# Kernel optimization log

Measured on AMD Instinct MI355X. Metric: run time of the kernel, lower is better.

## Reference

```python
import jax, jax.numpy as jnp
import numpy as np

C = 256  # hidden_channels
N = 262144  # number of nodes


def setup_inputs() -> dict:
    key = jax.random.key(0)
    ks = jax.random.split(key, 6)
    s = 1.0 / np.sqrt(C)
    return {
        "x": jax.random.normal(ks[0], (N, C), dtype=jnp.float32),
        "Wq": jax.random.uniform(ks[1], (C, C), jnp.float32, -s, s),
        "Wk": jax.random.uniform(ks[2], (C, C), jnp.float32, -s, s),
        "Wv": jax.random.uniform(ks[3], (C, C), jnp.float32, -s, s),
        "Wo": jax.random.uniform(ks[4], (C, C), jnp.float32, -s, s),
        "bo": jax.random.uniform(ks[5], (C,), jnp.float32, -s, s),
    }


def reference(x, Wq, Wk, Wv, Wo, bo):
    # torch nn.Linear: y = x @ W.T
    q = jax.nn.elu(x @ Wq.T) + 1.0          # [N, C], strictly positive feature map
    k = jax.nn.elu(x @ Wk.T) + 1.0          # [N, C]
    v = x @ Wv.T                             # [N, C]
    kv = k.T @ v                             # [C, C] aggregate
    z = 1.0 / jnp.maximum(q @ k.sum(axis=0), 1e-6)  # [N] normalizer
    h = (q @ kv) * z[:, None]                # [N, C]
    # dropout p=0.0 (and eval mode) -> identity
    return h @ Wo.T + bo
```

## Files before the change

### kernel.cpp

```cpp
#include <hip/hip_runtime.h>
#include <cstdint>


typedef __attribute__((ext_vector_type(8))) short short8;
typedef __attribute__((ext_vector_type(4))) float f32x4;
typedef unsigned short u16;
typedef unsigned int u32;

#define MFMA16(a, b, c) __builtin_amdgcn_mfma_f32_16x16x32_bf16(a, b, c, 0, 0, 0)

__device__ __forceinline__ u32 bf16_1(float f) {
  u32 u = __float_as_uint(f);
  return (u + 0x7FFFu + ((u >> 16) & 1u)) >> 16;
}
__device__ __forceinline__ u32 bf16pk(float lo, float hi) {
  return bf16_1(lo) | (bf16_1(hi) << 16);
}

__global__ void prep_kernel(const float* __restrict__ Wq, const float* __restrict__ Wk,
                            const float* __restrict__ Wv, u16* __restrict__ WqF,
                            u16* __restrict__ WkF, u16* __restrict__ WvF,
                            float* __restrict__ kvp, float* __restrict__ ksum, int P) {
  int id = blockIdx.x * 256 + threadIdx.x;
  if (id < 256) ksum[id] = 0.f;
  for (int t = id; t < 3 * 65536; t += 65536) {
    int mat = t >> 16;
    int e = t & 65535;
    int c = e >> 8, d = e & 255;
    const float* src = (mat == 0) ? Wq : (mat == 1) ? Wk : Wv;
    u16* dst = (mat == 0) ? WqF : (mat == 1) ? WkF : WvF;
    int idx = (((c >> 5) * 8 + (d >> 5)) * 2 + ((c >> 4) & 1)) * 512 +
              ((d >> 3) & 3) * 128 + (c & 15) * 8 + (d & 7);
    dst[idx] = (u16)bf16_1(src[e]);
  }
  if (P < 256) {
    float4 z4 = {0.f, 0.f, 0.f, 0.f};
    float4* kz = (float4*)kvp;
    int total = P * 16384;
    for (int t = id; t < total; t += 65536) kz[t] = z4;
  }
}

__global__ __launch_bounds__(512, 2) void phase1_kernel(
    const float* __restrict__ x, const u16* __restrict__ WkF,
    const u16* __restrict__ WvF, float* __restrict__ kvp, float* __restrict__ ksum,
    int P) {
  __shared__ __align__(16) u16 xv_l[16384];
  __shared__ __align__(16) u16 kT_l[16384];
  const int tid = threadIdx.x;
  const int lane = tid & 63;
  const int w = tid >> 6;
  const int m = lane & 15;
  const int q = lane >> 4;
  const int wg = blockIdx.x;

  const f32x4 fz = {0.f, 0.f, 0.f, 0.f};
  f32x4 kvacc[16][2];
#pragma unroll
  for (int tr = 0; tr < 16; ++tr) {
    kvacc[tr][0] = fz;
    kvacc[tr][1] = fz;
  }
  float ksl0 = 0.f, ksl1 = 0.f;

  for (int it = 0; it < 16; ++it) {
    const int row0 = wg * 1024 + it * 64;
    __syncthreads();
    {
      const int r = tid >> 3, a = tid & 7;
      const float4* xp = (const float4*)(x + (size_t)(row0 + r) * 256 + a * 32);
#pragma unroll
      for (int i = 0; i < 8; ++i) {
        float4 f = xp[i];
        int db = 4 * a + (i >> 1);
        int pos = db * 512 + ((r ^ (db & 7)) << 3) + 4 * (i & 1);
        uint2 v;
        v.x = bf16pk(f.x, f.y);
        v.y = bf16pk(f.z, f.w);
        *(uint2*)&xv_l[pos] = v;
      }
    }
    __syncthreads();
    f32x4 kacc[4][2], vacc[4][2];
#pragma unroll
    for (int rt = 0; rt < 4; ++rt) {
      kacc[rt][0] = fz; kacc[rt][1] = fz;
      vacc[rt][0] = fz; vacc[rt][1] = fz;
    }
#pragma unroll
    for (int ks = 0; ks < 8; ++ks) {
      const int fb = ((w * 8 + ks) * 2) * 512 + lane * 8;
      short8 wk0 = *(const short8*)(WkF + fb);
      short8 wk1 = *(const short8*)(WkF + fb + 512);
      short8 wv0 = *(const short8*)(WvF + fb);
      short8 wv1 = *(const short8*)(WvF + fb + 512);
      const int db = 4 * ks + q;
      const int sw = db & 7;
#pragma unroll
      for (int rt = 0; rt < 4; ++rt) {
        int r = 16 * rt + m;
        short8 af = *(const short8*)&xv_l[db * 512 + ((r ^ sw) << 3)];
        kacc[rt][0] = MFMA16(af, wk0, kacc[rt][0]);
        kacc[rt][1] = MFMA16(af, wk1, kacc[rt][1]);
        vacc[rt][0] = MFMA16(af, wv0, vacc[rt][0]);
        vacc[rt][1] = MFMA16(af, wv1, vacc[rt][1]);
      }
    }
    __syncthreads();
#pragma unroll
    for (int rt = 0; rt < 4; ++rt) {
#pragma unroll
      for (int ct = 0; ct < 2; ++ct) {
        f32x4 kk = kacc[rt][ct];
        float e0 = kk[0] > 0.f ? kk[0] + 1.f : __expf(kk[0]);
        float e1 = kk[1] > 0.f ? kk[1] + 1.f : __expf(kk[1]);
        float e2 = kk[2] > 0.f ? kk[2] + 1.f : __expf(kk[2]);
        float e3 = kk[3] > 0.f ? kk[3] + 1.f : __expf(kk[3]);
        if (ct == 0) ksl0 += (e0 + e1) + (e2 + e3);
        else         ksl1 += (e0 + e1) + (e2 + e3);
        int col = 32 * w + 16 * ct + m;
        int pos = (2 * rt + (q >> 1)) * 2048 + col * 8 + 4 * (q & 1);
        uint2 kp;
        kp.x = bf16pk(e0, e1);
        kp.y = bf16pk(e2, e3);
        *(uint2*)&kT_l[pos] = kp;
        f32x4 vv = vacc[rt][ct];
        uint2 vp;
        vp.x = bf16pk(vv[0], vv[1]);
        vp.y = bf16pk(vv[2], vv[3]);
        *(uint2*)&xv_l[pos] = vp;
      }
    }
    __syncthreads();
#pragma unroll
    for (int kc = 0; kc < 2; ++kc) {
      const int rbb = (4 * kc + q) * 2048;
      short8 bf0 = *(const short8*)&xv_l[rbb + (32 * w + m) * 8];
      short8 bf1 = *(const short8*)&xv_l[rbb + (32 * w + 16 + m) * 8];
#pragma unroll
      for (int tr = 0; tr < 16; ++tr) {
        short8 af = *(const short8*)&kT_l[rbb + (16 * tr + m) * 8];
        kvacc[tr][0] = MFMA16(af, bf0, kvacc[tr][0]);
        kvacc[tr][1] = MFMA16(af, bf1, kvacc[tr][1]);
      }
    }
  }
  float s0 = ksl0, s1 = ksl1;
  s0 += __shfl_xor(s0, 16); s0 += __shfl_xor(s0, 32);
  s1 += __shfl_xor(s1, 16); s1 += __shfl_xor(s1, 32);
  if (q == 0) {
    atomicAdd(&ksum[32 * w + m], s0);
    atomicAdd(&ksum[32 * w + 16 + m], s1);
  }
  float* dst = kvp + (size_t)((P == 256) ? wg : (wg & (P - 1))) * 65536;
  if (P == 256) {
#pragma unroll
    for (int tr = 0; tr < 16; ++tr)
#pragma unroll
      for (int ct = 0; ct < 2; ++ct)
#pragma unroll
        for (int e = 0; e < 4; ++e) {
          int i = 16 * tr + 4 * q + e;
          int j = 32 * w + 16 * ct + m;
          dst[i * 256 + j] = kvacc[tr][ct][e];
        }
  } else {
#pragma unroll
    for (int tr = 0; tr < 16; ++tr)
#pragma unroll
      for (int ct = 0; ct < 2; ++ct)
#pragma unroll
        for (int e = 0; e < 4; ++e) {
          int i = 16 * tr + 4 * q + e;
          int j = 32 * w + 16 * ct + m;
          atomicAdd(&dst[i * 256 + j], kvacc[tr][ct][e]);
        }
  }
}

__global__ void mid1_kernel(const float* __restrict__ kvp, float* __restrict__ kv_red,
                            int P) {
  int id = blockIdx.x * 512 + threadIdx.x;
  float s = 0.f;
  for (int p = 0; p < P; ++p) s += kvp[(size_t)p * 65536 + id];
  kv_red[id] = s;
}

__global__ void mid2_kernel(const float* __restrict__ kv_red,
                            const float* __restrict__ Wo, u16* __restrict__ MF) {
  __shared__ float kr[256];
  const int i = blockIdx.x;
  const int j = threadIdx.x;
  kr[j] = kv_red[i * 256 + j];
  __syncthreads();
  float acc = 0.f;
  const float* wo = Wo + (size_t)j * 256;
#pragma unroll 8
  for (int c = 0; c < 256; ++c) acc += kr[c] * wo[c];
  MF[(((j >> 5) * 8 + (i >> 5)) * 2 + ((j >> 4) & 1)) * 512 + ((i >> 3) & 3) * 128 +
     (j & 15) * 8 + (i & 7)] = (u16)bf16_1(acc);
}

__global__ __launch_bounds__(512, 2) void phase2_kernel(
    const float* __restrict__ x, const u16* __restrict__ WqF,
    const u16* __restrict__ MF, const float* __restrict__ ksum,
    const float* __restrict__ bo, float* __restrict__ out) {
  __shared__ __align__(16) u16 xq_l[16384];
  __shared__ float s_l[64];
  const int tid = threadIdx.x;
  const int lane = tid & 63;
  const int w = tid >> 6;
  const int m = lane & 15;
  const int q = lane >> 4;
  const int wg = blockIdx.x;
  const f32x4 fz = {0.f, 0.f, 0.f, 0.f};

  short8 mf[8][2];
#pragma unroll
  for (int ks = 0; ks < 8; ++ks) {
    mf[ks][0] = *(const short8*)(MF + ((w * 8 + ks) * 2) * 512 + lane * 8);
    mf[ks][1] = *(const short8*)(MF + ((w * 8 + ks) * 2 + 1) * 512 + lane * 8);
  }
  const float ks0 = ksum[32 * w + m];
  const float ks1 = ksum[32 * w + 16 + m];
  const float b0 = bo[32 * w + m];
  const float b1 = bo[32 * w + 16 + m];

  for (int it = 0; it < 16; ++it) {
    const int row0 = wg * 1024 + it * 64;
    __syncthreads();
    {
      const int r = tid >> 3, a = tid & 7;
      const float4* xp = (const float4*)(x + (size_t)(row0 + r) * 256 + a * 32);
#pragma unroll
      for (int i = 0; i < 8; ++i) {
        float4 f = xp[i];
        int db = 4 * a + (i >> 1);
        int pos = db * 512 + ((r ^ (db & 7)) << 3) + 4 * (i & 1);
        uint2 v;
        v.x = bf16pk(f.x, f.y);
        v.y = bf16pk(f.z, f.w);
        *(uint2*)&xq_l[pos] = v;
      }
      if (tid < 64) s_l[tid] = 0.f;
    }
    __syncthreads();
    f32x4 qacc[4][2];
#pragma unroll
    for (int rt = 0; rt < 4; ++rt) { qacc[rt][0] = fz; qacc[rt][1] = fz; }
#pragma unroll
    for (int ks = 0; ks < 8; ++ks) {
      const int fb = ((w * 8 + ks) * 2) * 512 + lane * 8;
      short8 wq0 = *(const short8*)(WqF + fb);
      short8 wq1 = *(const short8*)(WqF + fb + 512);
      const int db = 4 * ks + q;
      const int sw = db & 7;
#pragma unroll
      for (int rt = 0; rt < 4; ++rt) {
        int r = 16 * rt + m;
        short8 af = *(const short8*)&xq_l[db * 512 + ((r ^ sw) << 3)];
        qacc[rt][0] = MFMA16(af, wq0, qacc[rt][0]);
        qacc[rt][1] = MFMA16(af, wq1, qacc[rt][1]);
      }
    }
#pragma unroll
    for (int rt = 0; rt < 4; ++rt) {
#pragma unroll
      for (int ct = 0; ct < 2; ++ct) {
        f32x4 a = qacc[rt][ct];
        a[0] = a[0] > 0.f ? a[0] + 1.f : __expf(a[0]);
        a[1] = a[1] > 0.f ? a[1] + 1.f : __expf(a[1]);
        a[2] = a[2] > 0.f ? a[2] + 1.f : __expf(a[2]);
        a[3] = a[3] > 0.f ? a[3] + 1.f : __expf(a[3]);
        qacc[rt][ct] = a;
      }
#pragma unroll
      for (int e = 0; e < 4; ++e) {
        float val = qacc[rt][0][e] * ks0 + qacc[rt][1][e] * ks1;
        val += __shfl_xor(val, 1);
        val += __shfl_xor(val, 2);
        val += __shfl_xor(val, 4);
        val += __shfl_xor(val, 8);
        if (m == 0) atomicAdd(&s_l[16 * rt + 4 * q + e], val);
      }
    }
    __syncthreads();
#pragma unroll
    for (int rt = 0; rt < 4; ++rt)
#pragma unroll
      for (int ct = 0; ct < 2; ++ct) {
        int c = 32 * w + 16 * ct + m;
        int db = c >> 3;
        int sw = db & 7;
        int cw = c & 7;
#pragma unroll
        for (int e = 0; e < 4; ++e) {
          int r = 16 * rt + 4 * q + e;
          xq_l[db * 512 + ((r ^ sw) << 3) + cw] = (u16)bf16_1(qacc[rt][ct][e]);
        }
      }
    __syncthreads();
    f32x4 tacc[4][2];
#pragma unroll
    for (int rt = 0; rt < 4; ++rt) { tacc[rt][0] = fz; tacc[rt][1] = fz; }
#pragma unroll
    for (int ks = 0; ks < 8; ++ks) {
      const int db = 4 * ks + q;
      const int sw = db & 7;
#pragma unroll
      for (int rt = 0; rt < 4; ++rt) {
        int r = 16 * rt + m;
        short8 af = *(const short8*)&xq_l[db * 512 + ((r ^ sw) << 3)];
        tacc[rt][0] = MFMA16(af, mf[ks][0], tacc[rt][0]);
        tacc[rt][1] = MFMA16(af, mf[ks][1], tacc[rt][1]);
      }
    }
#pragma unroll
    for (int rt = 0; rt < 4; ++rt)
#pragma unroll
      for (int e = 0; e < 4; ++e) {
        int r = 16 * rt + 4 * q + e;
        float z = __builtin_amdgcn_rcpf(fmaxf(s_l[r], 1e-6f));
        float* op = out + (size_t)(row0 + r) * 256 + 32 * w;
        op[m] = tacc[rt][0][e] * z + b0;
        op[16 + m] = tacc[rt][1][e] * z + b1;
      }
  }
}

extern "C" void kernel_launch(void* const* d_in, const int* in_sizes, int n_in,
                              void* d_out, int out_size, void* d_ws, size_t ws_size,
                              hipStream_t stream) {
  const float* x = (const float*)d_in[0];
  const float* Wq = (const float*)d_in[1];
  const float* Wk = (const float*)d_in[2];
  const float* Wv = (const float*)d_in[3];
  const float* Wo = (const float*)d_in[4];
  const float* bo = (const float*)d_in[5];
  float* out = (float*)d_out;

  const size_t fixedB = 1024 + 262144 + 4 * 131072;
  int P = 256;
  while (P > 1 && (size_t)P * 262144 + fixedB > ws_size) P >>= 1;

  char* base = (char*)d_ws;
  float* kvp = (float*)base;
  float* ksum = (float*)(base + (size_t)P * 262144);
  float* kvred = ksum + 256;
  u16* MF = (u16*)(kvred + 65536);
  u16* WqF = MF + 65536;
  u16* WkF = WqF + 65536;
  u16* WvF = WkF + 65536;

  prep_kernel<<<256, 256, 0, stream>>>(Wq, Wk, Wv, WqF, WkF, WvF, kvp, ksum, P);
  phase1_kernel<<<256, 512, 0, stream>>>(x, WkF, WvF, kvp, ksum, P);
  mid1_kernel<<<128, 512, 0, stream>>>(kvp, kvred, P);
  mid2_kernel<<<256, 256, 0, stream>>>(kvred, Wo, MF);
  phase2_kernel<<<256, 512, 0, stream>>>(x, WqF, MF, ksum, bo, out);
}
```

Before: 907.0 us.

## Double threads per block, split columns per wave, prefetch x, vectorize reduction

Phase1 and phase2 now launch 1024 threads (16 waves) per block, each wave owning 16 output columns instead of 32, which halves per-thread accumulator registers and raises the number of waves available to hide latency. The x tile load is changed to fully coalesced float4 reads. Phase2 additionally prefetches the next x tile into registers while computing the current one. The workspace slot allocation is reworked into exclusive plus shared atomic slots, and the mid1 reduction is vectorized with float4. The risk is more barrier contention across 16 waves and bf16 weight fragments being re-read by more waves.

```diff
diff --git a/kernel.cpp b/kernel.cpp
--- a/kernel.cpp
+++ b/kernel.cpp
@@ -20,7 +20,8 @@
 __global__ void prep_kernel(const float* __restrict__ Wq, const float* __restrict__ Wk,
                             const float* __restrict__ Wv, u16* __restrict__ WqF,
                             u16* __restrict__ WkF, u16* __restrict__ WvF,
-                            float* __restrict__ kvp, float* __restrict__ ksum, int P) {
+                            float* __restrict__ kvp, float* __restrict__ ksum,
+                            int E, int S) {
   int id = blockIdx.x * 256 + threadIdx.x;
   if (id < 256) ksum[id] = 0.f;
   for (int t = id; t < 3 * 65536; t += 65536) {
@@ -33,18 +34,18 @@
               ((d >> 3) & 3) * 128 + (c & 15) * 8 + (d & 7);
     dst[idx] = (u16)bf16_1(src[e]);
   }
-  if (P < 256) {
+  if (S > 0) {
     float4 z4 = {0.f, 0.f, 0.f, 0.f};
-    float4* kz = (float4*)kvp;
-    int total = P * 16384;
+    float4* kz = (float4*)(kvp + (size_t)E * 65536);
+    int total = S * 16384;
     for (int t = id; t < total; t += 65536) kz[t] = z4;
   }
 }
 
-__global__ __launch_bounds__(512, 2) void phase1_kernel(
+__global__ __launch_bounds__(1024, 4) void phase1_kernel(
     const float* __restrict__ x, const u16* __restrict__ WkF,
     const u16* __restrict__ WvF, float* __restrict__ kvp, float* __restrict__ ksum,
-    int P) {
+    int E, int S) {
   __shared__ __align__(16) u16 xv_l[16384];
   __shared__ __align__(16) u16 kT_l[16384];
   const int tid = threadIdx.x;
@@ -55,135 +56,119 @@
   const int wg = blockIdx.x;
 
   const f32x4 fz = {0.f, 0.f, 0.f, 0.f};
-  f32x4 kvacc[16][2];
-#pragma unroll
-  for (int tr = 0; tr < 16; ++tr) {
-    kvacc[tr][0] = fz;
-    kvacc[tr][1] = fz;
-  }
-  float ksl0 = 0.f, ksl1 = 0.f;
+  f32x4 kvacc[16];
+#pragma unroll
+  for (int tr = 0; tr < 16; ++tr) kvacc[tr] = fz;
+  float ksl = 0.f;
+
+  const int fb0 = (((w >> 1) * 8) * 2 + (w & 1)) * 512 + lane * 8;
+  const int sdb = (tid & 63) >> 1;
+  const int ssw = sdb & 7;
+  const int scw = 4 * (tid & 1);
+  const int srb = tid >> 6;
+  const int col = 16 * w + m;
 
   for (int it = 0; it < 16; ++it) {
     const int row0 = wg * 1024 + it * 64;
     __syncthreads();
     {
-      const int r = tid >> 3, a = tid & 7;
-      const float4* xp = (const float4*)(x + (size_t)(row0 + r) * 256 + a * 32);
-#pragma unroll
-      for (int i = 0; i < 8; ++i) {
-        float4 f = xp[i];
-        int db = 4 * a + (i >> 1);
-        int pos = db * 512 + ((r ^ (db & 7)) << 3) + 4 * (i & 1);
-        uint2 v;
-        v.x = bf16pk(f.x, f.y);
-        v.y = bf16pk(f.z, f.w);
-        *(uint2*)&xv_l[pos] = v;
-      }
-    }
-    __syncthreads();
-    f32x4 kacc[4][2], vacc[4][2];
-#pragma unroll
-    for (int rt = 0; rt < 4; ++rt) {
-      kacc[rt][0] = fz; kacc[rt][1] = fz;
-      vacc[rt][0] = fz; vacc[rt][1] = fz;
-    }
+      const float4* xp = (const float4*)(x + (size_t)row0 * 256);
+      float4 f0 = xp[tid];
+      float4 f1 = xp[1024 + tid];
+      float4 f2 = xp[2048 + tid];
+      float4 f3 = xp[3072 + tid];
+      uint2 u;
+      u.x = bf16pk(f0.x, f0.y); u.y = bf16pk(f0.z, f0.w);
+      *(uint2*)&xv_l[sdb * 512 + (((srb) ^ ssw) << 3) + scw] = u;
+      u.x = bf16pk(f1.x, f1.y); u.y = bf16pk(f1.z, f1.w);
+      *(uint2*)&xv_l[sdb * 512 + (((16 + srb) ^ ssw) << 3) + scw] = u;
+      u.x = bf16pk(f2.x, f2.y); u.y = bf16pk(f2.z, f2.w);
+      *(uint2*)&xv_l[sdb * 512 + (((32 + srb) ^ ssw) << 3) + scw] = u;
+      u.x = bf16pk(f3.x, f3.y); u.y = bf16pk(f3.z, f3.w);
+      *(uint2*)&xv_l[sdb * 512 + (((48 + srb) ^ ssw) << 3) + scw] = u;
+    }
+    __syncthreads();
+    f32x4 kacc[4], vacc[4];
+#pragma unroll
+    for (int rt = 0; rt < 4; ++rt) { kacc[rt] = fz; vacc[rt] = fz; }
 #pragma unroll
     for (int ks = 0; ks < 8; ++ks) {
-      const int fb = ((w * 8 + ks) * 2) * 512 + lane * 8;
-      short8 wk0 = *(const short8*)(WkF + fb);
-      short8 wk1 = *(const short8*)(WkF + fb + 512);
-      short8 wv0 = *(const short8*)(WvF + fb);
-      short8 wv1 = *(const short8*)(WvF + fb + 512);
+      const int fb = fb0 + ks * 1024;
+      short8 wk = *(const short8*)(WkF + fb);
+      short8 wv = *(const short8*)(WvF + fb);
       const int db = 4 * ks + q;
       const int sw = db & 7;
+      const u16* xb = &xv_l[db * 512];
 #pragma unroll
       for (int rt = 0; rt < 4; ++rt) {
-        int r = 16 * rt + m;
-        short8 af = *(const short8*)&xv_l[db * 512 + ((r ^ sw) << 3)];
-        kacc[rt][0] = MFMA16(af, wk0, kacc[rt][0]);
-        kacc[rt][1] = MFMA16(af, wk1, kacc[rt][1]);
-        vacc[rt][0] = MFMA16(af, wv0, vacc[rt][0]);
-        vacc[rt][1] = MFMA16(af, wv1, vacc[rt][1]);
+        short8 af = *(const short8*)&xb[((16 * rt + m) ^ sw) << 3];
+        kacc[rt] = MFMA16(af, wk, kacc[rt]);
+        vacc[rt] = MFMA16(af, wv, vacc[rt]);
       }
     }
     __syncthreads();
 #pragma unroll
     for (int rt = 0; rt < 4; ++rt) {
-#pragma unroll
-      for (int ct = 0; ct < 2; ++ct) {
-        f32x4 kk = kacc[rt][ct];
-        float e0 = kk[0] > 0.f ? kk[0] + 1.f : __expf(kk[0]);
-        float e1 = kk[1] > 0.f ? kk[1] + 1.f : __expf(kk[1]);
-        float e2 = kk[2] > 0.f ? kk[2] + 1.f : __expf(kk[2]);
-        float e3 = kk[3] > 0.f ? kk[3] + 1.f : __expf(kk[3]);
-        if (ct == 0) ksl0 += (e0 + e1) + (e2 + e3);
-        else         ksl1 += (e0 + e1) + (e2 + e3);
-        int col = 32 * w + 16 * ct + m;
-        int pos = (2 * rt + (q >> 1)) * 2048 + col * 8 + 4 * (q & 1);
-        uint2 kp;
-        kp.x = bf16pk(e0, e1);
-        kp.y = bf16pk(e2, e3);
-        *(uint2*)&kT_l[pos] = kp;
-        f32x4 vv = vacc[rt][ct];
-        uint2 vp;
-        vp.x = bf16pk(vv[0], vv[1]);
-        vp.y = bf16pk(vv[2], vv[3]);
-        *(uint2*)&xv_l[pos] = vp;
-      }
+      f32x4 kk = kacc[rt];
+      float e0 = kk[0] > 0.f ? kk[0] + 1.f : __expf(kk[0]);
+      float e1 = kk[1] > 0.f ? kk[1] + 1.f : __expf(kk[1]);
+      float e2 = kk[2] > 0.f ? kk[2] + 1.f : __expf(kk[2]);
+      float e3 = kk[3] > 0.f ? kk[3] + 1.f : __expf(kk[3]);
+      ksl += (e0 + e1) + (e2 + e3);
+      int pos = (2 * rt + (q >> 1)) * 2048 + col * 8 + 4 * (q & 1);
+      uint2 kp;
+      kp.x = bf16pk(e0, e1);
+      kp.y = bf16pk(e2, e3);
+      *(uint2*)&kT_l[pos] = kp;
+      f32x4 vv = vacc[rt];
+      uint2 vp;
+      vp.x = bf16pk(vv[0], vv[1]);
+      vp.y = bf16pk(vv[2], vv[3]);
+      *(uint2*)&xv_l[pos] = vp;
     }
     __syncthreads();
 #pragma unroll
     for (int kc = 0; kc < 2; ++kc) {
       const int rbb = (4 * kc + q) * 2048;
-      short8 bf0 = *(const short8*)&xv_l[rbb + (32 * w + m) * 8];
-      short8 bf1 = *(const short8*)&xv_l[rbb + (32 * w + 16 + m) * 8];
+      short8 bf = *(const short8*)&xv_l[rbb + col * 8];
 #pragma unroll
       for (int tr = 0; tr < 16; ++tr) {
         short8 af = *(const short8*)&kT_l[rbb + (16 * tr + m) * 8];
-        kvacc[tr][0] = MFMA16(af, bf0, kvacc[tr][0]);
-        kvacc[tr][1] = MFMA16(af, bf1, kvacc[tr][1]);
-      }
-    }
-  }
-  float s0 = ksl0, s1 = ksl1;
-  s0 += __shfl_xor(s0, 16); s0 += __shfl_xor(s0, 32);
-  s1 += __shfl_xor(s1, 16); s1 += __shfl_xor(s1, 32);
-  if (q == 0) {
-    atomicAdd(&ksum[32 * w + m], s0);
-    atomicAdd(&ksum[32 * w + 16 + m], s1);
-  }
-  float* dst = kvp + (size_t)((P == 256) ? wg : (wg & (P - 1))) * 65536;
-  if (P == 256) {
+        kvacc[tr] = MFMA16(af, bf, kvacc[tr]);
+      }
+    }
+  }
+  float s = ksl;
+  s += __shfl_xor(s, 16);
+  s += __shfl_xor(s, 32);
+  if (q == 0) atomicAdd(&ksum[col], s);
+  const int slot = (wg < E) ? wg : (E + ((wg - E) & (S - 1)));
+  float* dst = kvp + (size_t)slot * 65536;
+  if (wg < E) {
 #pragma unroll
     for (int tr = 0; tr < 16; ++tr)
 #pragma unroll
-      for (int ct = 0; ct < 2; ++ct)
-#pragma unroll
-        for (int e = 0; e < 4; ++e) {
-          int i = 16 * tr + 4 * q + e;
-          int j = 32 * w + 16 * ct + m;
-          dst[i * 256 + j] = kvacc[tr][ct][e];
-        }
+      for (int e = 0; e < 4; ++e)
+        dst[(16 * tr + 4 * q + e) * 256 + col] = kvacc[tr][e];
   } else {
 #pragma unroll
     for (int tr = 0; tr < 16; ++tr)
 #pragma unroll
-      for (int ct = 0; ct < 2; ++ct)
-#pragma unroll
-        for (int e = 0; e < 4; ++e) {
-          int i = 16 * tr + 4 * q + e;
-          int j = 32 * w + 16 * ct + m;
-          atomicAdd(&dst[i * 256 + j], kvacc[tr][ct][e]);
-        }
+      for (int e = 0; e < 4; ++e)
+        atomicAdd(&dst[(16 * tr + 4 * q + e) * 256 + col], kvacc[tr][e]);
   }
 }
 
 __global__ void mid1_kernel(const float* __restrict__ kvp, float* __restrict__ kv_red,
-                            int P) {
-  int id = blockIdx.x * 512 + threadIdx.x;
-  float s = 0.f;
-  for (int p = 0; p < P; ++p) s += kvp[(size_t)p * 65536 + id];
-  kv_red[id] = s;
+                            int nslots) {
+  int id = blockIdx.x * 256 + threadIdx.x;
+  float4 s = {0.f, 0.f, 0.f, 0.f};
+  const float4* kp = (const float4*)kvp;
+  for (int p = 0; p < nslots; ++p) {
+    float4 v = kp[(size_t)p * 16384 + id];
+    s.x += v.x; s.y += v.y; s.z += v.z; s.w += v.w;
+  }
+  ((float4*)kv_red)[id] = s;
 }
 
 __global__ void mid2_kernel(const float* __restrict__ kv_red,
@@ -201,7 +186,7 @@
      (j & 15) * 8 + (i & 7)] = (u16)bf16_1(acc);
 }
 
-__global__ __launch_bounds__(512, 2) void phase2_kernel(
+__global__ __launch_bounds__(1024, 4) void phase2_kernel(
     const float* __restrict__ x, const u16* __restrict__ WqF,
     const u16* __restrict__ MF, const float* __restrict__ ksum,
     const float* __restrict__ bo, float* __restrict__ out) {
@@ -215,68 +200,71 @@
   const int wg = blockIdx.x;
   const f32x4 fz = {0.f, 0.f, 0.f, 0.f};
 
-  short8 mf[8][2];
-#pragma unroll
-  for (int ks = 0; ks < 8; ++ks) {
-    mf[ks][0] = *(const short8*)(MF + ((w * 8 + ks) * 2) * 512 + lane * 8);
-    mf[ks][1] = *(const short8*)(MF + ((w * 8 + ks) * 2 + 1) * 512 + lane * 8);
-  }
-  const float ks0 = ksum[32 * w + m];
-  const float ks1 = ksum[32 * w + 16 + m];
-  const float b0 = bo[32 * w + m];
-  const float b1 = bo[32 * w + 16 + m];
+  const int fb0 = (((w >> 1) * 8) * 2 + (w & 1)) * 512 + lane * 8;
+  short8 mf[8];
+#pragma unroll
+  for (int ks = 0; ks < 8; ++ks) mf[ks] = *(const short8*)(MF + fb0 + ks * 1024);
+  const float ks0 = ksum[16 * w + m];
+  const float b0 = bo[16 * w + m];
+
+  const int sdb = (tid & 63) >> 1;
+  const int ssw = sdb & 7;
+  const int scw = 4 * (tid & 1);
+  const int srb = tid >> 6;
+  const int cq = 16 * w + m;
+
+  float4 pf0, pf1, pf2, pf3;
+  {
+    const float4* xp = (const float4*)(x + (size_t)wg * 1024 * 256);
+    pf0 = xp[tid]; pf1 = xp[1024 + tid]; pf2 = xp[2048 + tid]; pf3 = xp[3072 + tid];
+  }
 
   for (int it = 0; it < 16; ++it) {
     const int row0 = wg * 1024 + it * 64;
     __syncthreads();
     {
-      const int r = tid >> 3, a = tid & 7;
-      const float4* xp = (const float4*)(x + (size_t)(row0 + r) * 256 + a * 32);
-#pragma unroll
-      for (int i = 0; i < 8; ++i) {
-        float4 f = xp[i];
-        int db = 4 * a + (i >> 1);
-        int pos = db * 512 + ((r ^ (db & 7)) << 3) + 4 * (i & 1);
-        uint2 v;
-        v.x = bf16pk(f.x, f.y);
-        v.y = bf16pk(f.z, f.w);
-        *(uint2*)&xq_l[pos] = v;
-      }
+      uint2 u;
+      u.x = bf16pk(pf0.x, pf0.y); u.y = bf16pk(pf0.z, pf0.w);
+      *(uint2*)&xq_l[sdb * 512 + (((srb) ^ ssw) << 3) + scw] = u;
+      u.x = bf16pk(pf1.x, pf1.y); u.y = bf16pk(pf1.z, pf1.w);
+      *(uint2*)&xq_l[sdb * 512 + (((16 + srb) ^ ssw) << 3) + scw] = u;
+      u.x = bf16pk(pf2.x, pf2.y); u.y = bf16pk(pf2.z, pf2.w);
+      *(uint2*)&xq_l[sdb * 512 + (((32 + srb) ^ ssw) << 3) + scw] = u;
+      u.x = bf16pk(pf3.x, pf3.y); u.y = bf16pk(pf3.z, pf3.w);
+      *(uint2*)&xq_l[sdb * 512 + (((48 + srb) ^ ssw) << 3) + scw] = u;
       if (tid < 64) s_l[tid] = 0.f;
     }
     __syncthreads();
-    f32x4 qacc[4][2];
-#pragma unroll
-    for (int rt = 0; rt < 4; ++rt) { qacc[rt][0] = fz; qacc[rt][1] = fz; }
+    if (it < 15) {
+      const float4* xp = (const float4*)(x + (size_t)(row0 + 64) * 256);
+      pf0 = xp[tid]; pf1 = xp[1024 + tid]; pf2 = xp[2048 + tid]; pf3 = xp[3072 + tid];
+    }
+    f32x4 qacc[4];
+#pragma unroll
+    for (int rt = 0; rt < 4; ++rt) qacc[rt] = fz;
 #pragma unroll
     for (int ks = 0; ks < 8; ++ks) {
-      const int fb = ((w * 8 + ks) * 2) * 512 + lane * 8;
-      short8 wq0 = *(const short8*)(WqF + fb);
-      short8 wq1 = *(const short8*)(WqF + fb + 512);
+      short8 wq = *(const short8*)(WqF + fb0 + ks * 1024);
       const int db = 4 * ks + q;
       const int sw = db & 7;
+      const u16* xb = &xq_l[db * 512];
 #pragma unroll
       for (int rt = 0; rt < 4; ++rt) {
-        int r = 16 * rt + m;
-        short8 af = *(const short8*)&xq_l[db * 512 + ((r ^ sw) << 3)];
-        qacc[rt][0] = MFMA16(af, wq0, qacc[rt][0]);
-        qacc[rt][1] = MFMA16(af, wq1, qacc[rt][1]);
+        short8 af = *(const short8*)&xb[((16 * rt + m) ^ sw) << 3];
+        qacc[rt] = MFMA16(af, wq, qacc[rt]);
       }
     }
 #pragma unroll
     for (int rt = 0; rt < 4; ++rt) {
-#pragma unroll
-      for (int ct = 0; ct < 2; ++ct) {
-        f32x4 a = qacc[rt][ct];
-        a[0] = a[0] > 0.f ? a[0] + 1.f : __expf(a[0]);
-        a[1] = a[1] > 0.f ? a[1] + 1.f : __expf(a[1]);
-        a[2] = a[2] > 0.f ? a[2] + 1.f : __expf(a[2]);
-        a[3] = a[3] > 0.f ? a[3] + 1.f : __expf(a[3]);
-        qacc[rt][ct] = a;
-      }
+      f32x4 a = qacc[rt];
+      a[0] = a[0] > 0.f ? a[0] + 1.f : __expf(a[0]);
+      a[1] = a[1] > 0.f ? a[1] + 1.f : __expf(a[1]);
+      a[2] = a[2] > 0.f ? a[2] + 1.f : __expf(a[2]);
+      a[3] = a[3] > 0.f ? a[3] + 1.f : __expf(a[3]);
+      qacc[rt] = a;
 #pragma unroll
       for (int e = 0; e < 4; ++e) {
-        float val = qacc[rt][0][e] * ks0 + qacc[rt][1][e] * ks1;
+        float val = a[e] * ks0;
         val += __shfl_xor(val, 1);
         val += __shfl_xor(val, 2);
         val += __shfl_xor(val, 4);
@@ -285,34 +273,29 @@
       }
     }
     __syncthreads();
-#pragma unroll
-    for (int rt = 0; rt < 4; ++rt)
-#pragma unroll
-      for (int ct = 0; ct < 2; ++ct) {
-        int c = 32 * w + 16 * ct + m;
-        int db = c >> 3;
-        int sw = db & 7;
-        int cw = c & 7;
+    {
+      const int dbq = cq >> 3, swq = dbq & 7, cwq = cq & 7;
+#pragma unroll
+      for (int rt = 0; rt < 4; ++rt)
 #pragma unroll
         for (int e = 0; e < 4; ++e) {
           int r = 16 * rt + 4 * q + e;
-          xq_l[db * 512 + ((r ^ sw) << 3) + cw] = (u16)bf16_1(qacc[rt][ct][e]);
+          xq_l[dbq * 512 + ((r ^ swq) << 3) + cwq] = (u16)bf16_1(qacc[rt][e]);
         }
-      }
-    __syncthreads();
-    f32x4 tacc[4][2];
-#pragma unroll
-    for (int rt = 0; rt < 4; ++rt) { tacc[rt][0] = fz; tacc[rt][1] = fz; }
+    }
+    __syncthreads();
+    f32x4 tacc[4];
+#pragma unroll
+    for (int rt = 0; rt < 4; ++rt) tacc[rt] = fz;
 #pragma unroll
     for (int ks = 0; ks < 8; ++ks) {
       const int db = 4 * ks + q;
       const int sw = db & 7;
+      const u16* xb = &xq_l[db * 512];
 #pragma unroll
       for (int rt = 0; rt < 4; ++rt) {
-        int r = 16 * rt + m;
-        short8 af = *(const short8*)&xq_l[db * 512 + ((r ^ sw) << 3)];
-        tacc[rt][0] = MFMA16(af, mf[ks][0], tacc[rt][0]);
-        tacc[rt][1] = MFMA16(af, mf[ks][1], tacc[rt][1]);
+        short8 af = *(const short8*)&xb[((16 * rt + m) ^ sw) << 3];
+        tacc[rt] = MFMA16(af, mf[ks], tacc[rt]);
       }
     }
 #pragma unroll
@@ -321,9 +304,7 @@
       for (int e = 0; e < 4; ++e) {
         int r = 16 * rt + 4 * q + e;
         float z = __builtin_amdgcn_rcpf(fmaxf(s_l[r], 1e-6f));
-        float* op = out + (size_t)(row0 + r) * 256 + 32 * w;
-        op[m] = tacc[rt][0][e] * z + b0;
-        op[16 + m] = tacc[rt][1][e] * z + b1;
+        out[(size_t)(row0 + r) * 256 + cq] = tacc[rt][e] * z + b0;
       }
   }
 }
@@ -340,21 +321,29 @@
   float* out = (float*)d_out;
 
   const size_t fixedB = 1024 + 262144 + 4 * 131072;
-  int P = 256;
-  while (P > 1 && (size_t)P * 262144 + fixedB > ws_size) P >>= 1;
+  long long avail = (long long)ws_size - (long long)fixedB;
+  int slots = avail > 0 ? (int)(avail / 262144) : 1;
+  if (slots < 1) slots = 1;
+  if (slots > 256) slots = 256;
+  int E, S;
+  if (slots >= 256) { E = 256; S = 0; }
+  else if (slots >= 8) { E = slots - 4; S = 4; }
+  else if (slots >= 2) { E = slots - 1; S = 1; }
+  else { E = 0; S = 1; }
+  const int nslots = E + S;
 
   char* base = (char*)d_ws;
   float* kvp = (float*)base;
-  float* ksum = (float*)(base + (size_t)P * 262144);
+  float* ksum = (float*)(base + (size_t)nslots * 262144);
   float* kvred = ksum + 256;
   u16* MF = (u16*)(kvred + 65536);
   u16* WqF = MF + 65536;
   u16* WkF = WqF + 65536;
   u16* WvF = WkF + 65536;
 
-  prep_kernel<<<256, 256, 0, stream>>>(Wq, Wk, Wv, WqF, WkF, WvF, kvp, ksum, P);
-  phase1_kernel<<<256, 512, 0, stream>>>(x, WkF, WvF, kvp, ksum, P);
-  mid1_kernel<<<128, 512, 0, stream>>>(kvp, kvred, P);
+  prep_kernel<<<256, 256, 0, stream>>>(Wq, Wk, Wv, WqF, WkF, WvF, kvp, ksum, E, S);
+  phase1_kernel<<<256, 1024, 0, stream>>>(x, WkF, WvF, kvp, ksum, E, S);
+  mid1_kernel<<<64, 256, 0, stream>>>(kvp, kvred, nslots);
   mid2_kernel<<<256, 256, 0, stream>>>(kvred, Wo, MF);
-  phase2_kernel<<<256, 512, 0, stream>>>(x, WqF, MF, ksum, bo, out);
-}
+  phase2_kernel<<<256, 1024, 0, stream>>>(x, WqF, MF, ksum, bo, out);
+}
```

New measurement: 1.047 ms. +15.4%, slower.
